# Optimization experiments

Hardware: AMD Instinct MI355X
Metric: run time of the kernel (lower is better)

## Reference

```python
import jax, jax.numpy as jnp
import numpy as np

# ---- config (matches init_kwargs) ----
D_MODEL = 1024
D_STATE = 16
D_CONV = 4
EXPAND = 2
HEADDIM = 32
NGROUPS = 1
CHUNK = 256
D_INNER = EXPAND * D_MODEL            # 2048
NHEADS = D_INNER // HEADDIM           # 64
D_IN_PROJ = 2 * D_INNER + 2 * NGROUPS * D_STATE + NHEADS  # 4176
CONV_DIM = D_INNER + 2 * NGROUPS * D_STATE                # 2080
BATCH, SEQLEN = 2, 2048
EPS = 1e-5
NEG_INF = -1e9


def setup_inputs() -> dict:
    key = jax.random.key(0)
    ks = jax.random.split(key, 8)
    u = jax.random.normal(ks[0], (BATCH, SEQLEN, D_MODEL), jnp.float32)
    W_in = jax.random.normal(ks[1], (D_IN_PROJ, D_MODEL), jnp.float32) * (1.0 / np.sqrt(D_MODEL))
    conv_w = jax.random.normal(ks[2], (CONV_DIM, 1, D_CONV), jnp.float32) * (1.0 / np.sqrt(D_CONV))
    conv_b = jnp.zeros((CONV_DIM,), jnp.float32)
    dt_bias = jax.random.normal(ks[3], (NHEADS,), jnp.float32) * 0.1
    A_log = jnp.log(1.0 + 15.0 * jax.random.uniform(ks[4], (NHEADS,), jnp.float32))  # A in [1,16]
    D = jnp.ones((NHEADS,), jnp.float32)
    norm_w = jnp.ones((D_INNER,), jnp.float32)
    W_out = jax.random.normal(ks[5], (D_MODEL, D_INNER), jnp.float32) * (1.0 / np.sqrt(D_INNER))
    return dict(u=u, W_in=W_in, conv_w=conv_w, conv_b=conv_b, dt_bias=dt_bias,
                A_log=A_log, D=D, norm_w=norm_w, W_out=W_out)


def _ssd_chunk_scan(x, dt, A, Bm, Cm, Dh):
    """Mamba2 SSD chunked scan.
    x: (b,l,h,p), dt: (b,l,h), A: (h,), Bm/Cm: (b,l,n) [ngroups=1], Dh: (h,).
    """
    b, l, h, p = x.shape
    c = l // CHUNK
    n = Bm.shape[-1]
    xdt = x * dt[..., None]                                  # (b,l,h,p)
    xc = xdt.reshape(b, c, CHUNK, h, p)
    xo = x.reshape(b, c, CHUNK, h, p)
    Bc = Bm.reshape(b, c, CHUNK, n)
    Cc = Cm.reshape(b, c, CHUNK, n)
    Abar = (dt * A).reshape(b, c, CHUNK, h).transpose(0, 3, 1, 2)   # (b,h,c,l)
    Acum = jnp.cumsum(Abar, axis=-1)                                # (b,h,c,l)
    # intra-chunk decay matrix L[i,j] = exp(sum_{j<k<=i} Abar_k), causal
    seg = Acum[..., :, None] - Acum[..., None, :]                   # (b,h,c,l,l)
    causal = jnp.tril(jnp.ones((CHUNK, CHUNK), bool))
    Lmat = jnp.exp(jnp.where(causal, seg, NEG_INF))
    # diagonal (intra-chunk) contribution
    Yd = jnp.einsum('bcln,bcsn,bhcls,bcshp->bclhp', Cc, Bc, Lmat, xc)
    # chunk states
    decay_states = jnp.exp(Acum[..., -1:] - Acum)                   # (b,h,c,l)
    states = jnp.einsum('bcln,bhcl,bclhp->bchpn', Bc, decay_states, xc)
    chunk_decay = jnp.exp(Acum[..., -1])                            # (b,h,c)
    # inter-chunk recurrence over the c axis
    def step(carry, inp):
        s, dec = inp
        new = dec[..., None, None] * carry + s
        return new, carry
    s_t = jnp.moveaxis(states, 1, 0)            # (c,b,h,p,n)
    d_t = jnp.moveaxis(chunk_decay, -1, 0)      # (c,b,h)
    init = jnp.zeros((b, h, p, n), x.dtype)
    _, prev = jax.lax.scan(step, init, (s_t, d_t))
    prev = jnp.moveaxis(prev, 0, 1)             # (b,c,h,p,n) state entering each chunk
    Yo = jnp.einsum('bcln,bchpn,bhcl->bclhp', Cc, prev, jnp.exp(Acum))
    Y = Yd + Yo + xo * Dh[None, None, None, :, None]
    return Y.reshape(b, l, h, p)


def reference(u, W_in, conv_w, conv_b, dt_bias, A_log, D, norm_w, W_out):
    b, l, _ = u.shape
    zxbcdt = u @ W_in.T                                   # (b,l,D_IN_PROJ)
    z = zxbcdt[..., :D_INNER]
    xBC = zxbcdt[..., D_INNER:D_INNER + CONV_DIM]
    dt = jax.nn.softplus(zxbcdt[..., -NHEADS:] + dt_bias)  # (b,l,h)
    # depthwise causal conv1d + SiLU
    xBC_t = xBC.transpose(0, 2, 1)                        # (b, CONV_DIM, l)
    conv = jax.lax.conv_general_dilated(
        xBC_t, conv_w, window_strides=(1,), padding=[(D_CONV - 1, 0)],
        feature_group_count=CONV_DIM)
    xBC = jax.nn.silu(conv + conv_b[None, :, None]).transpose(0, 2, 1)
    x = xBC[..., :D_INNER]
    Bm = xBC[..., D_INNER:D_INNER + NGROUPS * D_STATE]
    Cm = xBC[..., D_INNER + NGROUPS * D_STATE:]
    A = -jnp.exp(A_log)
    Y = _ssd_chunk_scan(x.reshape(b, l, NHEADS, HEADDIM), dt, A, Bm, Cm, D)
    y = Y.reshape(b, l, D_INNER)
    # gated RMSNorm (norm_before_gate=False): normalize(y * silu(z)) * w
    yg = y * jax.nn.silu(z)
    yn = yg * jax.lax.rsqrt(jnp.mean(yg * yg, axis=-1, keepdims=True) + EPS) * norm_w
    out = yn @ W_out.T
    return (out, z)
```

## Files before the change

### kernel.cpp

```cpp
#include <hip/hip_runtime.h>

#define BATCH   2
#define SEQLEN  2048
#define DMODEL  1024
#define DINNER  2048
#define NHEADS  64
#define HEADDIM 32
#define DSTATE  16
#define CONVDIM 2080
#define DINPROJ 4192
#define NPAD    4224
#define CHUNK   256
#define NCHUNK  8
#define BL      (BATCH*SEQLEN)
#define XWIDTH  2144

typedef float  f4    __attribute__((ext_vector_type(4)));
typedef short  s16x8 __attribute__((ext_vector_type(8)));
typedef __bf16 bf16x8 __attribute__((ext_vector_type(8)));
typedef float  f32x4v __attribute__((ext_vector_type(4)));

#define MFMA16(a,b,c) __builtin_amdgcn_mfma_f32_16x16x32_bf16((a),(b),(c),0,0,0)

__device__ __forceinline__ unsigned short f2bf(float f){
  unsigned int u = __float_as_uint(f);
  u += 0x7FFFu + ((u >> 16) & 1u);
  return (unsigned short)(u >> 16);
}

__device__ __forceinline__ void gload_lds16(const void* g, void* l){
  __builtin_amdgcn_global_load_lds((const __attribute__((address_space(1))) unsigned int*)g,
                                   (__attribute__((address_space(3))) unsigned int*)l,
                                   16, 0, 0);
}

__device__ __forceinline__ bf16x8 f32x8_to_frag(const float* src, bool valid){
  bf16x8 r;
  if (valid) {
    f4 a = *(const f4*)src;
    f4 c = *(const f4*)(src + 4);
    r[0]=(__bf16)a[0]; r[1]=(__bf16)a[1]; r[2]=(__bf16)a[2]; r[3]=(__bf16)a[3];
    r[4]=(__bf16)c[0]; r[5]=(__bf16)c[1]; r[6]=(__bf16)c[2]; r[7]=(__bf16)c[3];
  } else {
    r[0]=(__bf16)0.f; r[1]=(__bf16)0.f; r[2]=(__bf16)0.f; r[3]=(__bf16)0.f;
    r[4]=(__bf16)0.f; r[5]=(__bf16)0.f; r[6]=(__bf16)0.f; r[7]=(__bf16)0.f;
  }
  return r;
}

__global__ void cast_f32_bf16(const float* __restrict__ in, unsigned short* __restrict__ out, int n){
  int i = blockIdx.x * 256 + threadIdx.x;
  if (i < n) out[i] = f2bf(in[i]);
}

__global__ void cast_win_pad(const float* __restrict__ in, unsigned short* __restrict__ out){
  int i = blockIdx.x * 256 + threadIdx.x;
  if (i >= NPAD * DMODEL) return;
  int r = i >> 10;
  out[i] = (r < DINPROJ) ? f2bf(in[i]) : (unsigned short)0;
}

template<int MODE>
__global__ __launch_bounds__(256) void gemm_bf16(
    const unsigned short* __restrict__ A,
    const unsigned short* __restrict__ B,
    int K, float* __restrict__ C0, float* __restrict__ C1, int N)
{
  __shared__ unsigned short As[2][128][32];
  __shared__ unsigned short Bs[2][128][32];

  const int nx   = gridDim.x;
  const int flat = blockIdx.y * nx + blockIdx.x;
  const int q    = (nx * gridDim.y) >> 3;
  const int swz  = (flat & 7) * q + (flat >> 3);
  const int bm   = swz / nx, bn = swz % nx;

  const int tid  = threadIdx.x;
  const int wave = tid >> 6, lane = tid & 63;
  const int wm   = (wave >> 1) * 64, wn = (wave & 1) * 64;
  const int lrow = lane & 15, khalf = lane >> 4;
  const int cswz = (khalf ^ (lrow & 3)) * 8;

  const int srow = wave * 16 + (lane >> 2);
  const int scol = (((lane & 3) ^ ((lane >> 2) & 3))) * 8;
  const unsigned short* Ag = A + (size_t)(bm * 128 + srow) * K + scol;
  const unsigned short* Bg = B + (size_t)(bn * 128 + srow) * K + scol;
  const int lr0 = wave * 16;

  f32x4v acc[4][4];
  #pragma unroll
  for (int i = 0; i < 4; ++i)
    #pragma unroll
    for (int j = 0; j < 4; ++j)
      acc[i][j] = (f32x4v){0.f,0.f,0.f,0.f};

  auto stage = [&](int buf, int k0){
    gload_lds16(Ag + k0,                   &As[buf][lr0][0]);
    gload_lds16(Ag + k0 + (size_t)64 * K,  &As[buf][64 + lr0][0]);
    gload_lds16(Bg + k0,                   &Bs[buf][lr0][0]);
    gload_lds16(Bg + k0 + (size_t)64 * K,  &Bs[buf][64 + lr0][0]);
  };

  const int NT = K >> 5;
  stage(0, 0);
  __syncthreads();
  for (int t = 0; t < NT; ++t) {
    const int cur = t & 1;
    if (t + 1 < NT) stage(cur ^ 1, (t + 1) << 5);
    bf16x8 af[4], bfr[4];
    #pragma unroll
    for (int i = 0; i < 4; ++i) {
      af[i]  = *(const bf16x8*)&As[cur][wm + i * 16 + lrow][cswz];
      bfr[i] = *(const bf16x8*)&Bs[cur][wn + i * 16 + lrow][cswz];
    }
    #pragma unroll
    for (int mi = 0; mi < 4; ++mi)
      #pragma unroll
      for (int ni = 0; ni < 4; ++ni)
        acc[mi][ni] = MFMA16(af[mi], bfr[ni], acc[mi][ni]);
    if (t + 1 < NT) __syncthreads();
  }

  const int orow0 = bm * 128 + wm;
  const int ocol0 = bn * 128 + wn;
  #pragma unroll
  for (int mi = 0; mi < 4; ++mi)
    #pragma unroll
    for (int ni = 0; ni < 4; ++ni) {
      int col  = ocol0 + ni * 16 + (lane & 15);
      int rowb = orow0 + mi * 16 + (lane >> 4) * 4;
      #pragma unroll
      for (int r = 0; r < 4; ++r) {
        int row = rowb + r;
        float v = acc[mi][ni][r];
        if (MODE == 0) {
          if (col < DINNER)        C0[(size_t)row * DINNER + col] = v;
          else if (col < DINPROJ)  C1[(size_t)row * XWIDTH + (col - DINNER)] = v;
        } else {
          C0[(size_t)row * N + col] = v;
        }
      }
    }
}

__global__ void conv_dt_kernel(const float* __restrict__ xbcdt,
                               const float* __restrict__ conv_w, const float* __restrict__ conv_b,
                               const float* __restrict__ dt_bias,
                               float* __restrict__ xconv, float* __restrict__ dtout)
{
  int idx = blockIdx.x * 256 + threadIdx.x;
  if (idx >= BL * XWIDTH) return;
  int ch = idx % XWIDTH;
  int bl = idx / XWIDTH;
  int l  = bl & (SEQLEN - 1);
  if (ch < CONVDIM) {
    float acc = conv_b[ch];
    #pragma unroll
    for (int j = 0; j < 4; ++j) {
      int ls = l - 3 + j;
      float x = (ls >= 0) ? xbcdt[(size_t)(bl - 3 + j) * XWIDTH + ch] : 0.f;
      acc += conv_w[ch * 4 + j] * x;
    }
    float s = acc / (1.f + __expf(-acc));
    xconv[(size_t)bl * CONVDIM + ch] = s;
  } else {
    int h = ch - CONVDIM;
    float x = xbcdt[(size_t)bl * XWIDTH + ch] + dt_bias[h];
    float dtv = (x > 20.f) ? x : log1pf(__expf(x));
    dtout[bl * NHEADS + h] = dtv;
  }
}

__global__ __launch_bounds__(256) void ssd_phaseA(
    const float* __restrict__ xconv, const float* __restrict__ dt,
    const float* __restrict__ A_log,
    float* __restrict__ acum, float* __restrict__ decay, float* __restrict__ states)
{
  int bc = blockIdx.x, h = blockIdx.y;
  int b = bc >> 3;
  int t = threadIdx.x;
  __shared__ float sAc[256], sCoef[256], sDt[256];
  __shared__ float sB[256][16];
  __shared__ float sX[256][32];
  int rowbase = b * SEQLEN + (bc & 7) * CHUNK;
  float dtv = dt[(rowbase + t) * NHEADS + h];
  float Av  = -__expf(A_log[h]);
  sAc[t] = dtv * Av; sDt[t] = dtv;
  for (int i = t; i < 256 * 16; i += 256) { int l = i >> 4, n = i & 15; sB[l][n] = xconv[(size_t)(rowbase + l) * CONVDIM + DINNER + n]; }
  for (int i = t; i < 256 * 32; i += 256) { int l = i >> 5, p = i & 31; sX[l][p] = xconv[(size_t)(rowbase + l) * CONVDIM + h * 32 + p]; }
  __syncthreads();
  for (int off = 1; off < 256; off <<= 1) {
    float add = (t >= off) ? sAc[t - off] : 0.f;
    __syncthreads();
    sAc[t] += add;
    __syncthreads();
  }
  int bch = bc * 64 + h;
  acum[(size_t)bch * 256 + t] = sAc[t];
  float last = sAc[255];
  if (t == 0) decay[bch] = __expf(last);
  sCoef[t] = sDt[t] * __expf(last - sAc[t]);
  __syncthreads();
  #pragma unroll
  for (int o = 0; o < 2; ++o) {
    int oi = t + o * 256;
    int p = oi >> 4, n = oi & 15;
    float acc = 0.f;
    for (int l = 0; l < 256; ++l) acc += sCoef[l] * sB[l][n] * sX[l][p];
    states[(size_t)bch * 512 + oi] = acc;
  }
}

__global__ void ssd_phaseB(const float* __restrict__ states, const float* __restrict__ decay,
                           float* __restrict__ prev)
{
  int bh = blockIdx.x;
  int b = bh >> 6, h = bh & 63;
  int t = threadIdx.x;
  float carry = 0.f;
  for (int c = 0; c < NCHUNK; ++c) {
    int bch = (b * 8 + c) * 64 + h;
    size_t base = (size_t)bch * 512 + t;
    prev[base] = carry;
    carry = decay[bch] * carry + states[base];
  }
}

__global__ __launch_bounds__(256, 2) void ssd_phaseC_mfma(
    const float* __restrict__ xconv, const float* __restrict__ dt,
    const float* __restrict__ acum, const float* __restrict__ prev,
    const float* __restrict__ Dvec, float* __restrict__ y)
{
  const int bc = blockIdx.x, h = blockIdx.y;
  const int b = bc >> 3;
  const int rowbase = b * SEQLEN + (bc & 7) * CHUNK;
  const int bch = bc * 64 + h;
  const int tid = threadIdx.x, wave = tid >> 6, lane = tid & 63;
  const int l16 = lane & 15, khalf = lane >> 4;

  __shared__ float sAcum[256];
  __shared__ __bf16 sXT[32][264];
  __shared__ __bf16 sP[4][2][16][40];

  if (tid < 256) sAcum[tid] = acum[(size_t)bch * 256 + tid];
  {
    int l  = tid >> 3;
    int p0 = (tid & 7) * 4;
    #pragma unroll
    for (int pass = 0; pass < 8; ++pass) {
      int ls = l + pass * 32;
      const float* xr = xconv + (size_t)(rowbase + ls) * CONVDIM + h * 32 + p0;
      f4 v = *(const f4*)xr;
      float dtl = dt[(rowbase + ls) * NHEADS + h];
      #pragma unroll
      for (int j = 0; j < 4; ++j) sXT[p0 + j][ls] = (__bf16)(v[j] * dtl);
    }
  }

  const bool kv = (khalf < 2);
  bf16x8 bfr[16], cfr[4], pvf[2];
  #pragma unroll
  for (int i = 0; i < 16; ++i)
    bfr[i] = f32x8_to_frag(xconv + (size_t)(rowbase + i * 16 + l16) * CONVDIM + DINNER + khalf * 8, kv);
  #pragma unroll
  for (int t = 0; t < 4; ++t)
    cfr[t] = f32x8_to_frag(xconv + (size_t)(rowbase + (wave + 4 * t) * 16 + l16) * CONVDIM + DINNER + DSTATE + khalf * 8, kv);
  #pragma unroll
  for (int pt = 0; pt < 2; ++pt)
    pvf[pt] = f32x8_to_frag(prev + (size_t)bch * 512 + (pt * 16 + l16) * 16 + khalf * 8, kv);
  __syncthreads();

  const float Dh = Dvec[h];
  #pragma unroll
  for (int t = 0; t < 4; ++t) {
    const int LT = wave + 4 * t;
    const int lbase = LT * 16;
    float al[4], el[4];
    #pragma unroll
    for (int r = 0; r < 4; ++r) { al[r] = sAcum[lbase + khalf * 4 + r]; el[r] = __expf(al[r]); }
    f32x4v y0 = MFMA16(cfr[t], pvf[0], ((f32x4v){0.f,0.f,0.f,0.f}));
    f32x4v y1 = MFMA16(cfr[t], pvf[1], ((f32x4v){0.f,0.f,0.f,0.f}));
    #pragma unroll
    for (int r = 0; r < 4; ++r) { y0[r] *= el[r]; y1[r] *= el[r]; }

    #pragma unroll
    for (int kp = 0; kp < 8; ++kp) {
      if (2 * kp <= LT) {
        f32x4v s0 = MFMA16(cfr[t], bfr[2 * kp],     ((f32x4v){0.f,0.f,0.f,0.f}));
        f32x4v s1 = MFMA16(cfr[t], bfr[2 * kp + 1], ((f32x4v){0.f,0.f,0.f,0.f}));
        const int buf = kp & 1;
        #pragma unroll
        for (int r = 0; r < 4; ++r) {
          int l  = lbase + khalf * 4 + r;
          int sA = 2 * kp * 16 + l16;
          int sB2 = sA + 16;
          float p0 = (sA  <= l) ? s0[r] * __expf(al[r] - sAcum[sA])  : 0.f;
          float p1 = (sB2 <= l) ? s1[r] * __expf(al[r] - sAcum[sB2]) : 0.f;
          sP[wave][buf][khalf * 4 + r][l16]      = (__bf16)p0;
          sP[wave][buf][khalf * 4 + r][16 + l16] = (__bf16)p1;
        }
        bf16x8 pa  = *(const bf16x8*)&sP[wave][buf][l16][khalf * 8];
        bf16x8 xf0 = *(const bf16x8*)&sXT[l16][kp * 32 + khalf * 8];
        bf16x8 xf1 = *(const bf16x8*)&sXT[16 + l16][kp * 32 + khalf * 8];
        y0 = MFMA16(pa, xf0, y0);
        y1 = MFMA16(pa, xf1, y1);
      }
    }

    #pragma unroll
    for (int r = 0; r < 4; ++r) {
      int lg = rowbase + lbase + khalf * 4 + r;
      const float* xr = xconv + (size_t)lg * CONVDIM + h * 32;
      float* yr = y + (size_t)lg * DINNER + h * 32;
      yr[l16]      = y0[r] + Dh * xr[l16];
      yr[16 + l16] = y1[r] + Dh * xr[16 + l16];
    }
  }
}

__global__ __launch_bounds__(256) void gate_norm(const float* __restrict__ y,
    const float* __restrict__ z, const float* __restrict__ norm_w,
    unsigned short* __restrict__ ynbf)
{
  int row = blockIdx.x, t = threadIdx.x;
  const float* yr = y + (size_t)row * DINNER;
  const float* zr = z + (size_t)row * DINNER;
  float vals[8];
  float ss = 0.f;
  #pragma unroll
  for (int i = 0; i < 8; ++i) {
    int ci = t + i * 256;
    float zv = zr[ci];
    float g = zv / (1.f + __expf(-zv));
    float v = yr[ci] * g;
    vals[i] = v; ss += v * v;
  }
  #pragma unroll
  for (int o = 1; o < 64; o <<= 1) ss += __shfl_xor(ss, o);
  __shared__ float sred[4];
  if ((t & 63) == 0) sred[t >> 6] = ss;
  __syncthreads();
  float tot = sred[0] + sred[1] + sred[2] + sred[3];
  float scale = rsqrtf(tot * (1.f / DINNER) + 1e-5f);
  #pragma unroll
  for (int i = 0; i < 8; ++i) {
    int ci = t + i * 256;
    ynbf[(size_t)row * DINNER + ci] = f2bf(vals[i] * scale * norm_w[ci]);
  }
}

extern "C" void kernel_launch(void* const* d_in, const int* in_sizes, int n_in,
                              void* d_out, int out_size, void* d_ws, size_t ws_size,
                              hipStream_t stream)
{
  const float* u       = (const float*)d_in[0];
  const float* W_in    = (const float*)d_in[1];
  const float* conv_w  = (const float*)d_in[2];
  const float* conv_b  = (const float*)d_in[3];
  const float* dt_bias = (const float*)d_in[4];
  const float* A_log   = (const float*)d_in[5];
  const float* Dv      = (const float*)d_in[6];
  const float* norm_w  = (const float*)d_in[7];
  const float* W_out   = (const float*)d_in[8];

  float* out  = (float*)d_out;
  float* zout = out + (size_t)BL * DMODEL;

  char* ws = (char*)d_ws;
  size_t off = 0;
  auto alloc = [&](size_t bytes){ size_t o = off; off += (bytes + 255) & ~(size_t)255; return o; };
  size_t o_ubf    = alloc((size_t)BL * DMODEL * 2);
  size_t o_wbf    = alloc((size_t)NPAD * DMODEL * 2);
  size_t o_xbcdt  = alloc((size_t)BL * XWIDTH * 4);
  size_t o_xconv  = alloc((size_t)BL * CONVDIM * 4);
  size_t o_dt     = alloc((size_t)BL * NHEADS * 4);
  size_t o_acum   = alloc((size_t)1024 * 256 * 4);
  size_t o_decay  = alloc((size_t)1024 * 4);
  size_t o_states = alloc((size_t)1024 * 512 * 4);
  size_t o_prev   = alloc((size_t)1024 * 512 * 4);
  size_t o_ynbf   = alloc((size_t)BL * DINNER * 2);

  unsigned short* ubf    = (unsigned short*)(ws + o_ubf);
  unsigned short* wbf    = (unsigned short*)(ws + o_wbf);
  float*          xbcdt  = (float*)(ws + o_xbcdt);
  float*          xconv  = (float*)(ws + o_xconv);
  float*          dtws   = (float*)(ws + o_dt);
  float*          acum   = (float*)(ws + o_acum);
  float*          decay  = (float*)(ws + o_decay);
  float*          states = (float*)(ws + o_states);
  float*          prevb  = (float*)(ws + o_prev);
  unsigned short* ynbf   = (unsigned short*)(ws + o_ynbf);
  unsigned short* woutbf = ubf;
  float*          ywork  = xbcdt;

  cast_f32_bf16<<<(BL * DMODEL) / 256, 256, 0, stream>>>(u, ubf, BL * DMODEL);
  cast_win_pad<<<(NPAD * DMODEL) / 256, 256, 0, stream>>>(W_in, wbf);

  gemm_bf16<0><<<dim3(NPAD / 128, BL / 128), 256, 0, stream>>>(ubf, wbf, DMODEL, zout, xbcdt, 0);

  conv_dt_kernel<<<(BL * XWIDTH) / 256, 256, 0, stream>>>(xbcdt, conv_w, conv_b, dt_bias, xconv, dtws);

  ssd_phaseA<<<dim3(16, 64), 256, 0, stream>>>(xconv, dtws, A_log, acum, decay, states);
  ssd_phaseB<<<128, 512, 0, stream>>>(states, decay, prevb);
  ssd_phaseC_mfma<<<dim3(16, 64), 256, 0, stream>>>(xconv, dtws, acum, prevb, Dv, ywork);

  gate_norm<<<BL, 256, 0, stream>>>(ywork, zout, norm_w, ynbf);

  cast_f32_bf16<<<(DMODEL * DINNER) / 256, 256, 0, stream>>>(W_out, woutbf, DMODEL * DINNER);

  gemm_bf16<1><<<dim3(DMODEL / 128, BL / 128), 256, 0, stream>>>(ynbf, woutbf, DINNER, out, nullptr, DMODEL);
}
```

Measured before the change: 246.3 us.

## Deepen GEMM prefetch pipeline, retune LDS swizzle, store conv output as bf16

The bf16 GEMM now issues two stages of global-to-LDS loads up front. It waits with explicit vmcnt counters and raw barriers instead of __syncthreads, and raises wave priority around the MFMA block, so loads overlap compute more fully. The LDS XOR swizzle pattern is changed, likely to reduce bank conflicts. Separately, the conv/SiLU output buffer is stored as bf16 rather than fp32, which halves its memory traffic in the SSD kernels. The cost is reduced precision for x, B and C values and reliance on hand-counted waitcnt correctness.

```diff
diff --git a/kernel.cpp b/kernel.cpp
--- a/kernel.cpp
+++ b/kernel.cpp
@@ -15,10 +15,11 @@
 #define BL      (BATCH*SEQLEN)
 #define XWIDTH  2144
 
-typedef float  f4    __attribute__((ext_vector_type(4)));
-typedef short  s16x8 __attribute__((ext_vector_type(8)));
-typedef __bf16 bf16x8 __attribute__((ext_vector_type(8)));
-typedef float  f32x4v __attribute__((ext_vector_type(4)));
+typedef float          f4    __attribute__((ext_vector_type(4)));
+typedef short          s16x8 __attribute__((ext_vector_type(8)));
+typedef unsigned short u16x4 __attribute__((ext_vector_type(4)));
+typedef __bf16         bf16x8 __attribute__((ext_vector_type(8)));
+typedef float          f32x4v __attribute__((ext_vector_type(4)));
 
 #define MFMA16(a,b,c) __builtin_amdgcn_mfma_f32_16x16x32_bf16((a),(b),(c),0,0,0)
 
@@ -26,6 +27,9 @@
   unsigned int u = __float_as_uint(f);
   u += 0x7FFFu + ((u >> 16) & 1u);
   return (unsigned short)(u >> 16);
+}
+__device__ __forceinline__ float bf2f(unsigned short u){
+  return __uint_as_float(((unsigned int)u) << 16);
 }
 
 __device__ __forceinline__ void gload_lds16(const void* g, void* l){
@@ -48,6 +52,17 @@
   return r;
 }
 
+__device__ __forceinline__ bf16x8 bf16x8_load(const unsigned short* src, bool valid){
+  if (valid) {
+    s16x8 v = *(const s16x8*)src;
+    return *(bf16x8*)&v;
+  }
+  bf16x8 r;
+  r[0]=(__bf16)0.f; r[1]=(__bf16)0.f; r[2]=(__bf16)0.f; r[3]=(__bf16)0.f;
+  r[4]=(__bf16)0.f; r[5]=(__bf16)0.f; r[6]=(__bf16)0.f; r[7]=(__bf16)0.f;
+  return r;
+}
+
 __global__ void cast_f32_bf16(const float* __restrict__ in, unsigned short* __restrict__ out, int n){
   int i = blockIdx.x * 256 + threadIdx.x;
   if (i < n) out[i] = f2bf(in[i]);
@@ -79,10 +94,10 @@
   const int wave = tid >> 6, lane = tid & 63;
   const int wm   = (wave >> 1) * 64, wn = (wave & 1) * 64;
   const int lrow = lane & 15, khalf = lane >> 4;
-  const int cswz = (khalf ^ (lrow & 3)) * 8;
+  const int cread = (khalf ^ ((lrow >> 1) & 3)) * 8;
 
   const int srow = wave * 16 + (lane >> 2);
-  const int scol = (((lane & 3) ^ ((lane >> 2) & 3))) * 8;
+  const int scol = ((lane & 3) ^ ((lane >> 3) & 3)) * 8;
   const unsigned short* Ag = A + (size_t)(bm * 128 + srow) * K + scol;
   const unsigned short* Bg = B + (size_t)(bn * 128 + srow) * K + scol;
   const int lr0 = wave * 16;
@@ -103,22 +118,29 @@
 
   const int NT = K >> 5;
   stage(0, 0);
-  __syncthreads();
+  stage(1, 32);
   for (int t = 0; t < NT; ++t) {
     const int cur = t & 1;
-    if (t + 1 < NT) stage(cur ^ 1, (t + 1) << 5);
+    if (t + 1 < NT) { asm volatile("s_waitcnt vmcnt(4)" ::: "memory"); }
+    else            { asm volatile("s_waitcnt vmcnt(0)" ::: "memory"); }
+    __builtin_amdgcn_s_barrier();
+    __builtin_amdgcn_sched_barrier(0);
     bf16x8 af[4], bfr[4];
     #pragma unroll
     for (int i = 0; i < 4; ++i) {
-      af[i]  = *(const bf16x8*)&As[cur][wm + i * 16 + lrow][cswz];
-      bfr[i] = *(const bf16x8*)&Bs[cur][wn + i * 16 + lrow][cswz];
-    }
+      af[i]  = *(const bf16x8*)&As[cur][wm + i * 16 + lrow][cread];
+      bfr[i] = *(const bf16x8*)&Bs[cur][wn + i * 16 + lrow][cread];
+    }
+    __builtin_amdgcn_s_setprio(1);
     #pragma unroll
     for (int mi = 0; mi < 4; ++mi)
       #pragma unroll
       for (int ni = 0; ni < 4; ++ni)
         acc[mi][ni] = MFMA16(af[mi], bfr[ni], acc[mi][ni]);
-    if (t + 1 < NT) __syncthreads();
+    __builtin_amdgcn_s_setprio(0);
+    __builtin_amdgcn_s_barrier();
+    __builtin_amdgcn_sched_barrier(0);
+    if (t + 2 < NT) stage(cur, (t + 2) << 5);
   }
 
   const int orow0 = bm * 128 + wm;
@@ -127,8 +149,8 @@
   for (int mi = 0; mi < 4; ++mi)
     #pragma unroll
     for (int ni = 0; ni < 4; ++ni) {
-      int col  = ocol0 + ni * 16 + (lane & 15);
-      int rowb = orow0 + mi * 16 + (lane >> 4) * 4;
+      int col  = ocol0 + ni * 16 + lrow;
+      int rowb = orow0 + mi * 16 + khalf * 4;
       #pragma unroll
       for (int r = 0; r < 4; ++r) {
         int row = rowb + r;
@@ -146,7 +168,7 @@
 __global__ void conv_dt_kernel(const float* __restrict__ xbcdt,
                                const float* __restrict__ conv_w, const float* __restrict__ conv_b,
                                const float* __restrict__ dt_bias,
-                               float* __restrict__ xconv, float* __restrict__ dtout)
+                               unsigned short* __restrict__ xconv, float* __restrict__ dtout)
 {
   int idx = blockIdx.x * 256 + threadIdx.x;
   if (idx >= BL * XWIDTH) return;
@@ -162,7 +184,7 @@
       acc += conv_w[ch * 4 + j] * x;
     }
     float s = acc / (1.f + __expf(-acc));
-    xconv[(size_t)bl * CONVDIM + ch] = s;
+    xconv[(size_t)bl * CONVDIM + ch] = f2bf(s);
   } else {
     int h = ch - CONVDIM;
     float x = xbcdt[(size_t)bl * XWIDTH + ch] + dt_bias[h];
@@ -172,7 +194,7 @@
 }
 
 __global__ __launch_bounds__(256) void ssd_phaseA(
-    const float* __restrict__ xconv, const float* __restrict__ dt,
+    const unsigned short* __restrict__ xconv, const float* __restrict__ dt,
     const float* __restrict__ A_log,
     float* __restrict__ acum, float* __restrict__ decay, float* __restrict__ states)
 {
@@ -186,8 +208,8 @@
   float dtv = dt[(rowbase + t) * NHEADS + h];
   float Av  = -__expf(A_log[h]);
   sAc[t] = dtv * Av; sDt[t] = dtv;
-  for (int i = t; i < 256 * 16; i += 256) { int l = i >> 4, n = i & 15; sB[l][n] = xconv[(size_t)(rowbase + l) * CONVDIM + DINNER + n]; }
-  for (int i = t; i < 256 * 32; i += 256) { int l = i >> 5, p = i & 31; sX[l][p] = xconv[(size_t)(rowbase + l) * CONVDIM + h * 32 + p]; }
+  for (int i = t; i < 256 * 16; i += 256) { int l = i >> 4, n = i & 15; sB[l][n] = bf2f(xconv[(size_t)(rowbase + l) * CONVDIM + DINNER + n]); }
+  for (int i = t; i < 256 * 32; i += 256) { int l = i >> 5, p = i & 31; sX[l][p] = bf2f(xconv[(size_t)(rowbase + l) * CONVDIM + h * 32 + p]); }
   __syncthreads();
   for (int off = 1; off < 256; off <<= 1) {
     float add = (t >= off) ? sAc[t - off] : 0.f;
@@ -227,7 +249,7 @@
 }
 
 __global__ __launch_bounds__(256, 2) void ssd_phaseC_mfma(
-    const float* __restrict__ xconv, const float* __restrict__ dt,
+    const unsigned short* __restrict__ xconv, const float* __restrict__ dt,
     const float* __restrict__ acum, const float* __restrict__ prev,
     const float* __restrict__ Dvec, float* __restrict__ y)
 {
@@ -249,11 +271,11 @@
     #pragma unroll
     for (int pass = 0; pass < 8; ++pass) {
       int ls = l + pass * 32;
-      const float* xr = xconv + (size_t)(rowbase + ls) * CONVDIM + h * 32 + p0;
-      f4 v = *(const f4*)xr;
+      const unsigned short* xr = xconv + (size_t)(rowbase + ls) * CONVDIM + h * 32 + p0;
+      u16x4 v = *(const u16x4*)xr;
       float dtl = dt[(rowbase + ls) * NHEADS + h];
       #pragma unroll
-      for (int j = 0; j < 4; ++j) sXT[p0 + j][ls] = (__bf16)(v[j] * dtl);
+      for (int j = 0; j < 4; ++j) sXT[p0 + j][ls] = (__bf16)(bf2f(v[j]) * dtl);
     }
   }
 
@@ -261,10 +283,10 @@
   bf16x8 bfr[16], cfr[4], pvf[2];
   #pragma unroll
   for (int i = 0; i < 16; ++i)
-    bfr[i] = f32x8_to_frag(xconv + (size_t)(rowbase + i * 16 + l16) * CONVDIM + DINNER + khalf * 8, kv);
+    bfr[i] = bf16x8_load(xconv + (size_t)(rowbase + i * 16 + l16) * CONVDIM + DINNER + khalf * 8, kv);
   #pragma unroll
   for (int t = 0; t < 4; ++t)
-    cfr[t] = f32x8_to_frag(xconv + (size_t)(rowbase + (wave + 4 * t) * 16 + l16) * CONVDIM + DINNER + DSTATE + khalf * 8, kv);
+    cfr[t] = bf16x8_load(xconv + (size_t)(rowbase + (wave + 4 * t) * 16 + l16) * CONVDIM + DINNER + DSTATE + khalf * 8, kv);
   #pragma unroll
   for (int pt = 0; pt < 2; ++pt)
     pvf[pt] = f32x8_to_frag(prev + (size_t)bch * 512 + (pt * 16 + l16) * 16 + khalf * 8, kv);
@@ -310,10 +332,10 @@
     #pragma unroll
     for (int r = 0; r < 4; ++r) {
       int lg = rowbase + lbase + khalf * 4 + r;
-      const float* xr = xconv + (size_t)lg * CONVDIM + h * 32;
+      const unsigned short* xr = xconv + (size_t)lg * CONVDIM + h * 32;
       float* yr = y + (size_t)lg * DINNER + h * 32;
-      yr[l16]      = y0[r] + Dh * xr[l16];
-      yr[16 + l16] = y1[r] + Dh * xr[16 + l16];
+      yr[l16]      = y0[r] + Dh * bf2f(xr[l16]);
+      yr[16 + l16] = y1[r] + Dh * bf2f(xr[16 + l16]);
     }
   }
 }
@@ -372,7 +394,7 @@
   size_t o_ubf    = alloc((size_t)BL * DMODEL * 2);
   size_t o_wbf    = alloc((size_t)NPAD * DMODEL * 2);
   size_t o_xbcdt  = alloc((size_t)BL * XWIDTH * 4);
-  size_t o_xconv  = alloc((size_t)BL * CONVDIM * 4);
+  size_t o_xconv  = alloc((size_t)BL * CONVDIM * 2);
   size_t o_dt     = alloc((size_t)BL * NHEADS * 4);
   size_t o_acum   = alloc((size_t)1024 * 256 * 4);
   size_t o_decay  = alloc((size_t)1024 * 4);
@@ -383,7 +405,7 @@
   unsigned short* ubf    = (unsigned short*)(ws + o_ubf);
   unsigned short* wbf    = (unsigned short*)(ws + o_wbf);
   float*          xbcdt  = (float*)(ws + o_xbcdt);
-  float*          xconv  = (float*)(ws + o_xconv);
+  unsigned short* xconv  = (unsigned short*)(ws + o_xconv);
   float*          dtws   = (float*)(ws + o_dt);
   float*          acum   = (float*)(ws + o_acum);
   float*          decay  = (float*)(ws + o_decay);
```

Result: faster. 225.7 us (-8.4%).
